# Performance work log

Hardware: AMD Instinct MI355X
Metric: run time of the kernel (lower is better)

## Reference

```python
import jax, jax.numpy as jnp
import numpy as np

HIDDEN = 256

def setup_inputs() -> dict:
    key = jax.random.key(0)
    ks = jax.random.split(key, 8)
    B, N1, N2, D = 4, 4096, 4096, 256
    s = 1.0 / np.sqrt(D)
    return {
        "inputs1": jax.random.normal(ks[0], (B, N1, D), jnp.float32),
        "inputs2": jax.random.normal(ks[1], (B, N2, D), jnp.float32),
        "mask": jax.random.randint(ks[2], (B, N1, N2), 0, 2, jnp.int32),
        "Wq": jax.random.normal(ks[3], (D, HIDDEN), jnp.float32) * s,
        "bq": jnp.zeros((HIDDEN,), jnp.float32),
        "Wk": jax.random.normal(ks[4], (D, HIDDEN), jnp.float32) * s,
        "bk": jnp.zeros((HIDDEN,), jnp.float32),
        "Wv": jax.random.normal(ks[5], (D, HIDDEN), jnp.float32) * s,
        "bv": jnp.zeros((HIDDEN,), jnp.float32),
    }

def reference(inputs1, inputs2, mask, Wq, bq, Wk, bk, Wv, bv):
    # q: (B,N1,H), k,v: (B,N2,H)
    q = inputs1 @ Wq + bq
    k = inputs2 @ Wk + bk
    v = inputs2 @ Wv + bv
    scale = 1.0 / np.sqrt(HIDDEN)
    # scores: (B,N1,N2)
    scores = jnp.einsum('bnh,bmh->bnm', q, k) * scale
    # original: masked_fill(mask <= 0, 1e-9) -- NOT -inf; replicate faithfully
    scores = jnp.where(mask <= 0, jnp.float32(1e-9), scores)
    attn = jax.nn.softmax(scores, axis=-1)
    return jnp.einsum('bnm,bmh->bnh', attn, v)
```

## Files before the change

### kernel.cpp

```cpp
#include <hip/hip_runtime.h>

typedef float  f32x4 __attribute__((ext_vector_type(4)));
typedef short  s16x8 __attribute__((ext_vector_type(8)));
typedef short  s16x4 __attribute__((ext_vector_type(4)));

#define MFMA16(a,b,c) __builtin_amdgcn_mfma_f32_16x16x32_bf16(a,b,c,0,0,0)

static __device__ __forceinline__ f32x4 mfma_pv(s16x4 a, s16x4 b, f32x4 c){
#if defined(__HIP_DEVICE_COMPILE__)
    return __builtin_amdgcn_mfma_f32_16x16x16bf16_1k(a, b, c, 0, 0, 0);
#else
    (void)a; (void)b; return c;
#endif
}

static __device__ __forceinline__ unsigned short f2bf(float f){
    union { float f; unsigned int u; } x; x.f = f;
    unsigned int r = x.u + 0x7fffu + ((x.u >> 16) & 1u);
    return (unsigned short)(r >> 16);
}

__global__ void wt_prep(const float* __restrict__ Wq, const float* __restrict__ Wk,
                        const float* __restrict__ Wv, unsigned short* __restrict__ wt){
    int n = blockIdx.x, p = blockIdx.y, k = threadIdx.x;
    const float* W = (p==0) ? Wq : ((p==1) ? Wk : Wv);
    wt[p*65536 + n*256 + k] = f2bf(W[k*256 + n]);
}

static __device__ __forceinline__ void stage_x(const float* x, size_t row0,
                                               int tid, unsigned short* sX){
    const float* xg = x + row0*256;
    #pragma unroll
    for(int rr=0; rr<16; rr++){
        int c = tid + rr*256;
        int row = c>>6, cc = c&63;
        float4 f = *(const float4*)(xg + row*256 + cc*4);
        unsigned short* d = &sX[row*264 + cc*4];
        d[0]=f2bf(f.x); d[1]=f2bf(f.y); d[2]=f2bf(f.z); d[3]=f2bf(f.w);
    }
}

__global__ __launch_bounds__(256) void proj_all(const float* __restrict__ x1,
        const float* __restrict__ x2, const unsigned short* __restrict__ wt,
        const float* __restrict__ bq, const float* __restrict__ bk,
        const float* __restrict__ bv, int b0,
        unsigned short* __restrict__ qdst, unsigned short* __restrict__ kfrag,
        unsigned short* __restrict__ vfrag){
    const int rt = blockIdx.x, p = blockIdx.y, z = blockIdx.z;
    const int zz = b0 + z;
    const int tid = threadIdx.x, w = tid>>6, lane = tid&63, quad = lane>>4, lq = lane&15;
    __shared__ __align__(16) unsigned short sX[64*264];

    const float* x = (p==0) ? x1 : x2;
    stage_x(x, (size_t)(zz*64 + rt)*64, tid, sX);
    __syncthreads();

    s16x8 a[8];
    #pragma unroll
    for(int ks=0; ks<8; ks++)
        a[ks] = *(const s16x8*)(&sX[(16*w+lq)*264 + ks*32 + quad*8]);

    f32x4 acc[16];
    #pragma unroll
    for(int t=0;t<16;t++) acc[t] = (f32x4)(0.0f);
    const unsigned short* wtp = wt + p*65536;
    #pragma unroll
    for(int ks=0; ks<8; ks++){
        #pragma unroll
        for(int t=0; t<16; t++){
            s16x8 bf_ = *(const s16x8*)(wtp + (16*t+lq)*256 + ks*32 + quad*8);
            acc[t] = MFMA16(a[ks], bf_, acc[t]);
        }
    }

    if(p == 0){
        #pragma unroll
        for(int t=0;t<16;t++){
            float bvf = bq[16*t+lq];
            #pragma unroll
            for(int r=0;r<4;r++){
                size_t row = (size_t)(zz*64 + rt)*64 + 16*w + 4*quad + r;
                qdst[row*256 + 16*t + lq] = f2bf(acc[t][r] + bvf);
            }
        }
    } else if(p == 1){
        __syncthreads();
        #pragma unroll
        for(int t=0;t<16;t++){
            float bvf = bk[16*t+lq];
            #pragma unroll
            for(int r=0;r<4;r++)
                sX[(16*w + 4*quad + r)*264 + 16*t + lq] = f2bf(acc[t][r] + bvf);
        }
        __syncthreads();
        unsigned short* kd = kfrag + (size_t)z*1048576;
        #pragma unroll
        for(int ks=0; ks<8; ks++){
            s16x8 v = *(const s16x8*)(&sX[(16*w + lq)*264 + 32*ks + 8*quad]);
            *(s16x8*)(kd + ((((size_t)rt*4 + w)*8 + ks)*64 + lane)*8) = v;
        }
    } else {
        unsigned short* vd = vfrag + (size_t)z*1048576;
        #pragma unroll
        for(int t2=0; t2<8; t2++){
            float b0f = bv[16*(2*t2  )+lq];
            float b1f = bv[16*(2*t2+1)+lq];
            s16x8 o;
            #pragma unroll
            for(int r=0;r<4;r++){
                o[r]   = (short)f2bf(acc[2*t2  ][r] + b0f);
                o[4+r] = (short)f2bf(acc[2*t2+1][r] + b1f);
            }
            *(s16x8*)(vd + ((((size_t)rt*4 + w)*8 + t2)*64 + lane)*8) = o;
        }
    }
}

__global__ __launch_bounds__(512,2) void attn(
        const unsigned short* __restrict__ qb, const unsigned short* __restrict__ kfrag,
        const unsigned short* __restrict__ vfrag, const int* __restrict__ mask,
        float* __restrict__ out, int b0){
    const int bid = blockIdx.x;
    int b, qt, bk_;
    if(gridDim.x == 256){ b = (bid&7)>>1; qt = (bid>>3)*2 + (bid&1); bk_ = b; }
    else                { b = b0; qt = bid; bk_ = 0; }
    const int tid = threadIdx.x, w4 = tid>>6, lane = tid&63, quad = lane>>4, lq = lane&15;
    const int qg = w4>>2, w = w4&3;
    const int qbase = qt*64 + 32*qg;

    __shared__ float sRS[2][4][32];
    __shared__ float sRed[4][32*65 + 1];

    s16x8 qf[2][8];
    #pragma unroll
    for(int rg=0; rg<2; rg++){
        size_t row = (size_t)(b*4096 + qbase + 16*rg + lq);
        #pragma unroll
        for(int ks=0; ks<8; ks++)
            qf[rg][ks] = *(const s16x8*)(qb + row*256 + ks*32 + quad*8);
    }

    f32x4 oacc[16][2];
    #pragma unroll
    for(int t=0;t<16;t++){ oacc[t][0] = (f32x4)(0.0f); oacc[t][1] = (f32x4)(0.0f); }
    float rsum[2] = {0.0f, 0.0f};

    const unsigned short* kfb = kfrag + (size_t)bk_*1048576;
    const unsigned short* vfb = vfrag + (size_t)bk_*1048576;
    const int* mp0 = mask + ((size_t)(b*4096 + qbase) + lq)*4096 + 16*w + 4*quad;

    for(int kt=0; kt<64; kt++){
        const size_t fb = ((size_t)kt*4 + w)*8*64*8;
        s16x8 kf[8];
        #pragma unroll
        for(int ks=0; ks<8; ks++)
            kf[ks] = *(const s16x8*)(kfb + fb + ((size_t)ks*64 + lane)*8);
        int4 m0 = *(const int4*)(mp0 + (size_t)kt*64);
        int4 m1 = *(const int4*)(mp0 + (size_t)16*4096 + kt*64);
        f32x4 sacc0 = (f32x4)(0.0f), sacc1 = (f32x4)(0.0f);
        #pragma unroll
        for(int ks=0; ks<8; ks++){
            sacc0 = MFMA16(kf[ks], qf[0][ks], sacc0);
            sacc1 = MFMA16(kf[ks], qf[1][ks], sacc1);
        }
        s16x4 pb0, pb1;
        {
            float p;
            p = (m0.x>0)?__expf(sacc0[0]*0.0625f):1.0f; rsum[0]+=p; pb0[0]=(short)f2bf(p);
            p = (m0.y>0)?__expf(sacc0[1]*0.0625f):1.0f; rsum[0]+=p; pb0[1]=(short)f2bf(p);
            p = (m0.z>0)?__expf(sacc0[2]*0.0625f):1.0f; rsum[0]+=p; pb0[2]=(short)f2bf(p);
            p = (m0.w>0)?__expf(sacc0[3]*0.0625f):1.0f; rsum[0]+=p; pb0[3]=(short)f2bf(p);
            p = (m1.x>0)?__expf(sacc1[0]*0.0625f):1.0f; rsum[1]+=p; pb1[0]=(short)f2bf(p);
            p = (m1.y>0)?__expf(sacc1[1]*0.0625f):1.0f; rsum[1]+=p; pb1[1]=(short)f2bf(p);
            p = (m1.z>0)?__expf(sacc1[2]*0.0625f):1.0f; rsum[1]+=p; pb1[2]=(short)f2bf(p);
            p = (m1.w>0)?__expf(sacc1[3]*0.0625f):1.0f; rsum[1]+=p; pb1[3]=(short)f2bf(p);
        }
        #pragma unroll
        for(int t2=0; t2<8; t2++){
            s16x8 vv = *(const s16x8*)(vfb + fb + ((size_t)t2*64 + lane)*8);
            s16x4 vlo = __builtin_shufflevector(vv, vv, 0,1,2,3);
            s16x4 vhi = __builtin_shufflevector(vv, vv, 4,5,6,7);
            oacc[2*t2  ][0] = mfma_pv(vlo, pb0, oacc[2*t2  ][0]);
            oacc[2*t2  ][1] = mfma_pv(vlo, pb1, oacc[2*t2  ][1]);
            oacc[2*t2+1][0] = mfma_pv(vhi, pb0, oacc[2*t2+1][0]);
            oacc[2*t2+1][1] = mfma_pv(vhi, pb1, oacc[2*t2+1][1]);
        }
    }

    #pragma unroll
    for(int rg=0; rg<2; rg++){
        float v = rsum[rg];
        v += __shfl_xor(v, 16);
        v += __shfl_xor(v, 32);
        if(quad == 0) sRS[qg][w][16*rg + lq] = v;
    }

    for(int g=0; g<2; g++){
        for(int c=0; c<4; c++){
            __syncthreads();
            if(qg == g){
                #pragma unroll
                for(int tt=0; tt<4; tt++){
                    int t = 4*c + tt;
                    #pragma unroll
                    for(int rg=0; rg<2; rg++){
                        #pragma unroll
                        for(int r=0; r<4; r++)
                            sRed[w][(16*rg+lq)*65 + 16*tt + 4*quad + r] = oacc[t][rg][r];
                    }
                }
            }
            __syncthreads();
            #pragma unroll
            for(int j=0; j<4; j++){
                int idx = j*512 + tid;
                int hl = idx & 63, q = idx >> 6;
                float s  = sRed[0][q*65+hl] + sRed[1][q*65+hl]
                         + sRed[2][q*65+hl] + sRed[3][q*65+hl];
                float rs = sRS[g][0][q] + sRS[g][1][q] + sRS[g][2][q] + sRS[g][3][q];
                out[((size_t)(b*4096 + qt*64 + 32*g + q))*256 + 64*c + hl] = s / rs;
            }
        }
    }
}

extern "C" void kernel_launch(void* const* d_in, const int* in_sizes, int n_in,
                              void* d_out, int out_size, void* d_ws, size_t ws_size,
                              hipStream_t stream){
    (void)in_sizes; (void)n_in; (void)out_size;
    const float* x1 = (const float*)d_in[0];
    const float* x2 = (const float*)d_in[1];
    const int*   mk = (const int*)  d_in[2];
    const float* Wq = (const float*)d_in[3];
    const float* bq = (const float*)d_in[4];
    const float* Wk = (const float*)d_in[5];
    const float* bk = (const float*)d_in[6];
    const float* Wv = (const float*)d_in[7];
    const float* bv = (const float*)d_in[8];
    float* out = (float*)d_out;
    char* ws = (char*)d_ws;

    unsigned short* wt = (unsigned short*)ws;
    unsigned short* qb = (unsigned short*)(ws + 393216);
    const size_t kvoff = 393216 + 8388608;

    wt_prep<<<dim3(256,3), 256, 0, stream>>>(Wq, Wk, Wv, wt);

    if(ws_size >= kvoff + 16ull*1024*1024){
        unsigned short* kf = (unsigned short*)(ws + kvoff);
        unsigned short* vf = (unsigned short*)(ws + kvoff + 8388608);
        proj_all<<<dim3(64,3,4), 256, 0, stream>>>(x1, x2, wt, bq, bk, bv, 0,
                                                   qb, kf, vf);
        attn<<<256, 512, 0, stream>>>(qb, kf, vf, mk, out, 0);
    } else {
        unsigned short* kf = (unsigned short*)(ws + kvoff);
        unsigned short* vf = (unsigned short*)(ws + kvoff + 2097152);
        for(int b=0;b<4;b++){
            proj_all<<<dim3(64,3,1), 256, 0, stream>>>(x1, x2, wt, bq, bk, bv, b,
                                                       qb, kf, vf);
            attn<<<64, 512, 0, stream>>>(qb, kf, vf, mk, out, b);
        }
    }
}
```

Before: 616.1 us.

## Stage K/V fragments through double-buffered LDS with async global-to-LDS loads

The per-wave K and V fragment loads from global memory are replaced by cooperative global_load_lds copies into a 128KB double-buffered shared-memory region. The two query groups in a block now share each staged tile, and the next tile is prefetched while the current one is computed. The mask for the next tile is also loaded one iteration ahead. The cost is a block-wide barrier every key tile, and the large LDS footprint likely allows only one block per CU, halving occupancy.

New measurement: 563.5 us. 1.09x faster.

```diff
diff --git a/kernel.cpp b/kernel.cpp
--- a/kernel.cpp
+++ b/kernel.cpp
@@ -11,6 +11,16 @@
     return __builtin_amdgcn_mfma_f32_16x16x16bf16_1k(a, b, c, 0, 0, 0);
 #else
     (void)a; (void)b; return c;
+#endif
+}
+
+static __device__ __forceinline__ void glds16(const void* g, void* l){
+#if defined(__HIP_DEVICE_COMPILE__)
+    __builtin_amdgcn_global_load_lds(
+        (const __attribute__((address_space(1))) unsigned int*)g,
+        (__attribute__((address_space(3))) unsigned int*)l, 16, 0, 0);
+#else
+    (void)g; (void)l;
 #endif
 }
 
@@ -128,8 +138,7 @@
     const int qg = w4>>2, w = w4&3;
     const int qbase = qt*64 + 32*qg;
 
-    __shared__ float sRS[2][4][32];
-    __shared__ float sRed[4][32*65 + 1];
+    __shared__ __align__(16) unsigned char smem[131072];
 
     s16x8 qf[2][8];
     #pragma unroll
@@ -145,39 +154,48 @@
     for(int t=0;t<16;t++){ oacc[t][0] = (f32x4)(0.0f); oacc[t][1] = (f32x4)(0.0f); }
     float rsum[2] = {0.0f, 0.0f};
 
-    const unsigned short* kfb = kfrag + (size_t)bk_*1048576;
-    const unsigned short* vfb = vfrag + (size_t)bk_*1048576;
+    const unsigned char* kfb = (const unsigned char*)(kfrag + (size_t)bk_*1048576);
+    const unsigned char* vfb = (const unsigned char*)(vfrag + (size_t)bk_*1048576);
     const int* mp0 = mask + ((size_t)(b*4096 + qbase) + lq)*4096 + 16*w + 4*quad;
+    const unsigned lsl = w4*1024 + lane*16;
+    const unsigned ldd = w4*1024;
+
+    #pragma unroll
+    for(int r=0; r<4; r++){
+        glds16(kfb + r*8192 + lsl, smem + r*8192 + ldd);
+        glds16(vfb + r*8192 + lsl, smem + 32768 + r*8192 + ldd);
+    }
+    int4 mA0 = *(const int4*)(mp0);
+    int4 mA1 = *(const int4*)(mp0 + (size_t)16*4096);
 
     for(int kt=0; kt<64; kt++){
-        const size_t fb = ((size_t)kt*4 + w)*8*64*8;
-        s16x8 kf[8];
-        #pragma unroll
-        for(int ks=0; ks<8; ks++)
-            kf[ks] = *(const s16x8*)(kfb + fb + ((size_t)ks*64 + lane)*8);
-        int4 m0 = *(const int4*)(mp0 + (size_t)kt*64);
-        int4 m1 = *(const int4*)(mp0 + (size_t)16*4096 + kt*64);
+        const int cb = kt & 1;
+        __syncthreads();
+        const unsigned short* bK = (const unsigned short*)(smem + cb*65536);
+        const unsigned short* bV = (const unsigned short*)(smem + cb*65536 + 32768);
+
         f32x4 sacc0 = (f32x4)(0.0f), sacc1 = (f32x4)(0.0f);
         #pragma unroll
         for(int ks=0; ks<8; ks++){
-            sacc0 = MFMA16(kf[ks], qf[0][ks], sacc0);
-            sacc1 = MFMA16(kf[ks], qf[1][ks], sacc1);
+            s16x8 kf = *(const s16x8*)(bK + ((w*8 + ks)*64 + lane)*8);
+            sacc0 = MFMA16(kf, qf[0][ks], sacc0);
+            sacc1 = MFMA16(kf, qf[1][ks], sacc1);
         }
         s16x4 pb0, pb1;
         {
             float p;
-            p = (m0.x>0)?__expf(sacc0[0]*0.0625f):1.0f; rsum[0]+=p; pb0[0]=(short)f2bf(p);
-            p = (m0.y>0)?__expf(sacc0[1]*0.0625f):1.0f; rsum[0]+=p; pb0[1]=(short)f2bf(p);
-            p = (m0.z>0)?__expf(sacc0[2]*0.0625f):1.0f; rsum[0]+=p; pb0[2]=(short)f2bf(p);
-            p = (m0.w>0)?__expf(sacc0[3]*0.0625f):1.0f; rsum[0]+=p; pb0[3]=(short)f2bf(p);
-            p = (m1.x>0)?__expf(sacc1[0]*0.0625f):1.0f; rsum[1]+=p; pb1[0]=(short)f2bf(p);
-            p = (m1.y>0)?__expf(sacc1[1]*0.0625f):1.0f; rsum[1]+=p; pb1[1]=(short)f2bf(p);
-            p = (m1.z>0)?__expf(sacc1[2]*0.0625f):1.0f; rsum[1]+=p; pb1[2]=(short)f2bf(p);
-            p = (m1.w>0)?__expf(sacc1[3]*0.0625f):1.0f; rsum[1]+=p; pb1[3]=(short)f2bf(p);
+            p = (mA0.x>0)?__expf(sacc0[0]*0.0625f):1.0f; rsum[0]+=p; pb0[0]=(short)f2bf(p);
+            p = (mA0.y>0)?__expf(sacc0[1]*0.0625f):1.0f; rsum[0]+=p; pb0[1]=(short)f2bf(p);
+            p = (mA0.z>0)?__expf(sacc0[2]*0.0625f):1.0f; rsum[0]+=p; pb0[2]=(short)f2bf(p);
+            p = (mA0.w>0)?__expf(sacc0[3]*0.0625f):1.0f; rsum[0]+=p; pb0[3]=(short)f2bf(p);
+            p = (mA1.x>0)?__expf(sacc1[0]*0.0625f):1.0f; rsum[1]+=p; pb1[0]=(short)f2bf(p);
+            p = (mA1.y>0)?__expf(sacc1[1]*0.0625f):1.0f; rsum[1]+=p; pb1[1]=(short)f2bf(p);
+            p = (mA1.z>0)?__expf(sacc1[2]*0.0625f):1.0f; rsum[1]+=p; pb1[2]=(short)f2bf(p);
+            p = (mA1.w>0)?__expf(sacc1[3]*0.0625f):1.0f; rsum[1]+=p; pb1[3]=(short)f2bf(p);
         }
         #pragma unroll
         for(int t2=0; t2<8; t2++){
-            s16x8 vv = *(const s16x8*)(vfb + fb + ((size_t)t2*64 + lane)*8);
+            s16x8 vv = *(const s16x8*)(bV + ((w*8 + t2)*64 + lane)*8);
             s16x4 vlo = __builtin_shufflevector(vv, vv, 0,1,2,3);
             s16x4 vhi = __builtin_shufflevector(vv, vv, 4,5,6,7);
             oacc[2*t2  ][0] = mfma_pv(vlo, pb0, oacc[2*t2  ][0]);
@@ -185,16 +203,29 @@
             oacc[2*t2+1][0] = mfma_pv(vhi, pb0, oacc[2*t2+1][0]);
             oacc[2*t2+1][1] = mfma_pv(vhi, pb1, oacc[2*t2+1][1]);
         }
-    }
-
+        if(kt < 63){
+            const unsigned char* gK = kfb + (size_t)(kt+1)*32768;
+            const unsigned char* gV = vfb + (size_t)(kt+1)*32768;
+            unsigned char* dst = smem + (cb^1)*65536;
+            #pragma unroll
+            for(int r=0; r<4; r++){
+                glds16(gK + r*8192 + lsl, dst + r*8192 + ldd);
+                glds16(gV + r*8192 + lsl, dst + 32768 + r*8192 + ldd);
+            }
+            mA0 = *(const int4*)(mp0 + (size_t)(kt+1)*64);
+            mA1 = *(const int4*)(mp0 + (size_t)16*4096 + (kt+1)*64);
+        }
+    }
+
+    float* sRS  = (float*)smem;
+    float* sRed = (float*)(smem + 1024);
     #pragma unroll
     for(int rg=0; rg<2; rg++){
         float v = rsum[rg];
         v += __shfl_xor(v, 16);
         v += __shfl_xor(v, 32);
-        if(quad == 0) sRS[qg][w][16*rg + lq] = v;
-    }
-
+        if(quad == 0) sRS[(qg*4 + w)*32 + 16*rg + lq] = v;
+    }
     for(int g=0; g<2; g++){
         for(int c=0; c<4; c++){
             __syncthreads();
@@ -206,7 +237,7 @@
                     for(int rg=0; rg<2; rg++){
                         #pragma unroll
                         for(int r=0; r<4; r++)
-                            sRed[w][(16*rg+lq)*65 + 16*tt + 4*quad + r] = oacc[t][rg][r];
+                            sRed[w*2081 + (16*rg+lq)*65 + 16*tt + 4*quad + r] = oacc[t][rg][r];
                     }
                 }
             }
@@ -215,9 +246,10 @@
             for(int j=0; j<4; j++){
                 int idx = j*512 + tid;
                 int hl = idx & 63, q = idx >> 6;
-                float s  = sRed[0][q*65+hl] + sRed[1][q*65+hl]
-                         + sRed[2][q*65+hl] + sRed[3][q*65+hl];
-                float rs = sRS[g][0][q] + sRS[g][1][q] + sRS[g][2][q] + sRS[g][3][q];
+                float s  = sRed[0*2081 + q*65+hl] + sRed[1*2081 + q*65+hl]
+                         + sRed[2*2081 + q*65+hl] + sRed[3*2081 + q*65+hl];
+                float rs = sRS[(g*4+0)*32+q] + sRS[(g*4+1)*32+q]
+                         + sRS[(g*4+2)*32+q] + sRS[(g*4+3)*32+q];
                 out[((size_t)(b*4096 + qt*64 + 32*g + q))*256 + 64*c + hl] = s / rs;
             }
         }
```
